# Kernel optimization log

Hardware: AMD Instinct MI355X
Metric: run time of the kernel (lower is better)

The kernel has to match this reference:

```python
import jax, jax.numpy as jnp
import numpy as np

HIDDEN = 2048
N_HEADS = 32
N_KV = 8
HEAD_DIM = HIDDEN // N_HEADS  # 64
GROUP = N_HEADS // N_KV       # 4
FFN = 8192
EPS = 1e-5
ROPE_BASE = 500000.0
NEG = -1e9


def rms_norm(x, w, eps=EPS):
    var = jnp.mean(x * x, axis=-1, keepdims=True)
    return x * jax.lax.rsqrt(var + eps) * w


def rope_cos_sin(position_ids):
    # inv_freq: [head_dim//2]
    inv_freq = 1.0 / (ROPE_BASE ** (jnp.arange(0, HEAD_DIM, 2, dtype=jnp.float32) / HEAD_DIM))
    freqs = position_ids.astype(jnp.float32)[:, :, None] * inv_freq[None, None, :]  # [b,s,d/2]
    emb = jnp.concatenate([freqs, freqs], axis=-1)  # [b,s,d]
    return jnp.cos(emb), jnp.sin(emb)


def rotate_half(x):
    x1, x2 = jnp.split(x, 2, axis=-1)
    return jnp.concatenate([-x2, x1], axis=-1)


def setup_inputs() -> dict:
    key = jax.random.key(0)
    ks = jax.random.split(key, 12)
    b, s = 2, 1024
    scale_h = 1.0 / np.sqrt(HIDDEN)
    scale_f = 1.0 / np.sqrt(FFN)
    hidden_states = jax.random.normal(ks[0], (b, s, HIDDEN), jnp.float32)
    causal = jnp.where(jnp.tril(jnp.ones((s, s), bool)), 0.0, NEG).astype(jnp.float32)
    attention_mask = jnp.broadcast_to(causal[None, None], (b, 1, s, s))
    position_ids = jnp.broadcast_to(jnp.arange(s, dtype=jnp.int32)[None], (b, s))
    return {
        "hidden_states": hidden_states,
        "attention_mask": attention_mask,
        "wq": jax.random.normal(ks[1], (HIDDEN, N_HEADS * HEAD_DIM), jnp.float32) * scale_h,
        "wk": jax.random.normal(ks[2], (HIDDEN, N_KV * HEAD_DIM), jnp.float32) * scale_h,
        "wv": jax.random.normal(ks[3], (HIDDEN, N_KV * HEAD_DIM), jnp.float32) * scale_h,
        "wo": jax.random.normal(ks[4], (N_HEADS * HEAD_DIM, HIDDEN), jnp.float32) * scale_h,
        "norm1_w": jnp.ones((HIDDEN,), jnp.float32),
        "norm2_w": jnp.ones((HIDDEN,), jnp.float32),
        "w_gate": jax.random.normal(ks[5], (HIDDEN, FFN), jnp.float32) * scale_h,
        "w_up": jax.random.normal(ks[6], (HIDDEN, FFN), jnp.float32) * scale_h,
        "w_down": jax.random.normal(ks[7], (FFN, HIDDEN), jnp.float32) * scale_f,
        "position_ids": position_ids,
    }


def reference(hidden_states, attention_mask, wq, wk, wv, wo, norm1_w, norm2_w,
              w_gate, w_up, w_down, position_ids):
    b, s, _ = hidden_states.shape
    residual = hidden_states
    normed = rms_norm(hidden_states, norm1_w)

    q = (normed @ wq).reshape(b, s, N_HEADS, HEAD_DIM).transpose(0, 2, 1, 3)  # [b,H,s,d]
    k = (normed @ wk).reshape(b, s, N_KV, HEAD_DIM).transpose(0, 2, 1, 3)    # [b,G,s,d]
    v = (normed @ wv).reshape(b, s, N_KV, HEAD_DIM).transpose(0, 2, 1, 3)

    cos, sin = rope_cos_sin(position_ids)  # [b,s,d]
    cos, sin = cos[:, None], sin[:, None]  # unsqueeze head dim
    q = q * cos + rotate_half(q) * sin
    k = k * cos + rotate_half(k) * sin

    # repeat_kv: [b,G,s,d] -> [b,H,s,d]
    k = jnp.repeat(k, GROUP, axis=1)
    v = jnp.repeat(v, GROUP, axis=1)

    scores = jnp.einsum('bhqd,bhkd->bhqk', q, k)
    scores = scores + attention_mask  # mask added BEFORE scaling, as in source
    attn = jax.nn.softmax(scores / np.sqrt(HEAD_DIM), axis=-1)
    ctx = jnp.einsum('bhqk,bhkd->bhqd', attn, v)
    ctx = ctx.transpose(0, 2, 1, 3).reshape(b, s, N_HEADS * HEAD_DIM)
    attn_out = ctx @ wo

    normed_ff = rms_norm(attn_out + residual, norm2_w)
    ff = (jax.nn.silu(normed_ff @ w_gate) * (normed_ff @ w_up)) @ w_down
    return attn_out + ff
```

## Files before the change

### kernel.cpp

```cpp
#include <hip/hip_runtime.h>
#include <hip/hip_bf16.h>
#include <cstddef>
#include <cstdint>

#define T_TOK   2048
#define HID     2048
#define NHEADS  32
#define NKV     8
#define HDIM    64
#define FFN_DIM 8192
#define QKV_N   3072

typedef __hip_bfloat16 bf16;
typedef __attribute__((ext_vector_type(8))) short short8;
typedef __attribute__((ext_vector_type(4))) float f32x4;
typedef __attribute__((ext_vector_type(4))) unsigned short us4;

typedef __attribute__((address_space(1))) const void cg_void;
typedef __attribute__((address_space(3))) void lds_void;

__global__ __launch_bounds__(256) void cast_transpose(const float* __restrict__ in,
                                                      bf16* __restrict__ out,
                                                      int K, int N)
{
    __shared__ bf16 t[64][65];
    const int n0 = blockIdx.x * 64, k0 = blockIdx.y * 64;
    const int tn = threadIdx.x & 63, tk = threadIdx.x >> 6;
    #pragma unroll
    for (int kk = tk; kk < 64; kk += 4)
        t[kk][tn] = __float2bfloat16(in[(size_t)(k0 + kk) * N + n0 + tn]);
    __syncthreads();
    #pragma unroll
    for (int nn = tk; nn < 64; nn += 4)
        out[(size_t)(n0 + nn) * K + k0 + tn] = t[tn][nn];
}

__global__ __launch_bounds__(256) void cast_ilv(const float* __restrict__ in,
                                                bf16* __restrict__ out,
                                                int N, int is_up)
{
    __shared__ bf16 t[64][65];
    const int n0 = blockIdx.x * 64, k0 = blockIdx.y * 64;
    const int tn = threadIdx.x & 63, tk = threadIdx.x >> 6;
    #pragma unroll
    for (int kk = tk; kk < 64; kk += 4)
        t[kk][tn] = __float2bfloat16(in[(size_t)(k0 + kk) * N + n0 + tn]);
    __syncthreads();
    #pragma unroll
    for (int nn = tk; nn < 64; nn += 4) {
        int n = n0 + nn;
        int r = ((n >> 5) << 6) + (is_up << 5) + (n & 31);
        out[(size_t)r * HID + k0 + tn] = t[tn][nn];
    }
}

__global__ __launch_bounds__(256) void rmsnorm_kernel(const float* __restrict__ x,
                                                      const float* __restrict__ w,
                                                      bf16* __restrict__ out)
{
    __shared__ float sm[4];
    const int row = blockIdx.x, tid = threadIdx.x;
    const float4* xr = (const float4*)(x + (size_t)row * HID);
    float4 a = xr[tid], b = xr[tid + 256];
    float ss = a.x*a.x + a.y*a.y + a.z*a.z + a.w*a.w
             + b.x*b.x + b.y*b.y + b.z*b.z + b.w*b.w;
    #pragma unroll
    for (int off = 32; off; off >>= 1) ss += __shfl_down(ss, off);
    if ((tid & 63) == 0) sm[tid >> 6] = ss;
    __syncthreads();
    float sc = rsqrtf((sm[0] + sm[1] + sm[2] + sm[3]) * (1.0f / HID) + 1e-5f);
    const float4* wr = (const float4*)w;
    float4 w0 = wr[tid], w1 = wr[tid + 256];
    bf16* o = out + (size_t)row * HID;
    o[tid*4+0] = __float2bfloat16(a.x * sc * w0.x);
    o[tid*4+1] = __float2bfloat16(a.y * sc * w0.y);
    o[tid*4+2] = __float2bfloat16(a.z * sc * w0.z);
    o[tid*4+3] = __float2bfloat16(a.w * sc * w0.w);
    o[1024+tid*4+0] = __float2bfloat16(b.x * sc * w1.x);
    o[1024+tid*4+1] = __float2bfloat16(b.y * sc * w1.y);
    o[1024+tid*4+2] = __float2bfloat16(b.z * sc * w1.z);
    o[1024+tid*4+3] = __float2bfloat16(b.w * sc * w1.w);
}

__global__ __launch_bounds__(256) void rmsnorm_add_kernel(const float* __restrict__ xa,
                                                          const float* __restrict__ xb,
                                                          const float* __restrict__ w,
                                                          bf16* __restrict__ out)
{
    __shared__ float sm[4];
    const int row = blockIdx.x, tid = threadIdx.x;
    const float4* ar = (const float4*)(xa + (size_t)row * HID);
    const float4* br = (const float4*)(xb + (size_t)row * HID);
    float4 a0 = ar[tid], a1 = ar[tid + 256];
    float4 b0 = br[tid], b1 = br[tid + 256];
    float4 s0, s1;
    s0.x = a0.x + b0.x; s0.y = a0.y + b0.y; s0.z = a0.z + b0.z; s0.w = a0.w + b0.w;
    s1.x = a1.x + b1.x; s1.y = a1.y + b1.y; s1.z = a1.z + b1.z; s1.w = a1.w + b1.w;
    float ss = s0.x*s0.x + s0.y*s0.y + s0.z*s0.z + s0.w*s0.w
             + s1.x*s1.x + s1.y*s1.y + s1.z*s1.z + s1.w*s1.w;
    #pragma unroll
    for (int off = 32; off; off >>= 1) ss += __shfl_down(ss, off);
    if ((tid & 63) == 0) sm[tid >> 6] = ss;
    __syncthreads();
    float sc = rsqrtf((sm[0] + sm[1] + sm[2] + sm[3]) * (1.0f / HID) + 1e-5f);
    const float4* wr = (const float4*)w;
    float4 w0 = wr[tid], w1 = wr[tid + 256];
    bf16* o = out + (size_t)row * HID;
    o[tid*4+0] = __float2bfloat16(s0.x * sc * w0.x);
    o[tid*4+1] = __float2bfloat16(s0.y * sc * w0.y);
    o[tid*4+2] = __float2bfloat16(s0.z * sc * w0.z);
    o[tid*4+3] = __float2bfloat16(s0.w * sc * w0.w);
    o[1024+tid*4+0] = __float2bfloat16(s1.x * sc * w1.x);
    o[1024+tid*4+1] = __float2bfloat16(s1.y * sc * w1.y);
    o[1024+tid*4+2] = __float2bfloat16(s1.z * sc * w1.z);
    o[1024+tid*4+3] = __float2bfloat16(s1.w * sc * w1.w);
}

template<int BN>
__device__ __forceinline__ void gemm_body(
    const bf16* __restrict__ A, const bf16* __restrict__ Bt,
    float* __restrict__ Cf,
    int lda, int kbeg, int klen, int ldc, int bx, int by)
{
    constexpr int NFR   = BN / 32;
    constexpr int CALLS = 4 + NFR;
    constexpr int KSRD  = 4 + NFR;
    __shared__ bf16 As[2 * 128 * 64];
    __shared__ bf16 Bs[2 * BN * 64];
    const int tid = threadIdx.x;
    const int wv = tid >> 6, ln = tid & 63;
    const int wr = wv >> 1, wc = wv & 1;
    const size_t m0 = (size_t)by * 128;
    const size_t n0 = (size_t)bx * BN;

    const int lrow = ln >> 3;
    const int lk   = (ln & 7) ^ lrow;

    const bf16* Abase = A  + (m0 + (size_t)wv*32 + lrow) * lda + kbeg + lk*8;
    const bf16* Bbase = Bt + (n0 + (size_t)wv*NFR*8 + lrow) * lda + kbeg + lk*8;
    bf16* AsW = As + wv*2048;
    bf16* BsW = Bs + wv*NFR*512;

    auto stage = [&](int p, int tk) {
        #pragma unroll
        for (int i = 0; i < 4; ++i)
            __builtin_amdgcn_global_load_lds((cg_void*)(Abase + (size_t)i*8*lda + tk),
                                             (lds_void*)(AsW + p*8192 + i*512), 16, 0, 0);
        #pragma unroll
        for (int i = 0; i < NFR; ++i)
            __builtin_amdgcn_global_load_lds((cg_void*)(Bbase + (size_t)i*8*lda + tk),
                                             (lds_void*)(BsW + p*(BN*64) + i*512), 16, 0, 0);
    };

    f32x4 acc[4][NFR] = {};
    const int nt = klen >> 6;

    stage(0, 0);
    stage(1, 64);
    asm volatile("s_waitcnt vmcnt(%0)" :: "n"(CALLS) : "memory");
    __builtin_amdgcn_sched_barrier(0);
    __builtin_amdgcn_s_barrier();

    for (int t = 0; t < nt; ++t) {
        const int p = t & 1;
        const char* Ab = (const char*)As + p * 16384;
        const char* Bb = (const char*)Bs + p * (BN * 128);

        short8 af[4][2], bfr[NFR][2];
        #pragma unroll
        for (int ks = 0; ks < 2; ++ks) {
            const int kbyte = ks*64 + (ln >> 4)*16;
            #pragma unroll
            for (int m = 0; m < 4; ++m) {
                int row = wr*64 + m*16 + (ln & 15);
                af[m][ks] = *(const short8*)(Ab + row*128 + (kbyte ^ ((row & 7) << 4)));
            }
            #pragma unroll
            for (int n = 0; n < NFR; ++n) {
                int row = wc*(BN/2) + n*16 + (ln & 15);
                bfr[n][ks] = *(const short8*)(Bb + row*128 + (kbyte ^ ((row & 7) << 4)));
            }
        }
        asm volatile("s_waitcnt lgkmcnt(%0)" :: "n"(KSRD) : "memory");
        __builtin_amdgcn_sched_barrier(0);
        __builtin_amdgcn_s_setprio(1);
        #pragma unroll
        for (int m = 0; m < 4; ++m)
            #pragma unroll
            for (int n = 0; n < NFR; ++n)
                acc[m][n] = __builtin_amdgcn_mfma_f32_16x16x32_bf16(af[m][0], bfr[n][0], acc[m][n], 0, 0, 0);
        __builtin_amdgcn_s_setprio(0);
        asm volatile("s_waitcnt lgkmcnt(0)" ::: "memory");
        __builtin_amdgcn_sched_barrier(0);
        __builtin_amdgcn_s_barrier();

        const bool more = (t + 2 < nt);
        if (more) stage(p, (t + 2) * 64);
        __builtin_amdgcn_sched_barrier(0);

        __builtin_amdgcn_s_setprio(1);
        #pragma unroll
        for (int m = 0; m < 4; ++m)
            #pragma unroll
            for (int n = 0; n < NFR; ++n)
                acc[m][n] = __builtin_amdgcn_mfma_f32_16x16x32_bf16(af[m][1], bfr[n][1], acc[m][n], 0, 0, 0);
        __builtin_amdgcn_s_setprio(0);

        if (more) { asm volatile("s_waitcnt vmcnt(%0)" :: "n"(CALLS) : "memory"); }
        else      { asm volatile("s_waitcnt vmcnt(0)" ::: "memory"); }
        __builtin_amdgcn_sched_barrier(0);
        __builtin_amdgcn_s_barrier();
    }

    const int cj = ln & 15, rj = ln >> 4;
    #pragma unroll
    for (int m = 0; m < 4; ++m) {
        #pragma unroll
        for (int j = 0; j < 4; ++j) {
            size_t row = m0 + wr*64 + m*16 + rj*4 + j;
            #pragma unroll
            for (int n = 0; n < NFR; ++n) {
                int col = (int)n0 + wc*(BN/2) + n*16 + cj;
                Cf[row * (size_t)ldc + col] = acc[m][n][j];
            }
        }
    }
}

__device__ __forceinline__ void swz(int& bx, int& by) {
    const int nwg = gridDim.x * gridDim.y;
    int orig = blockIdx.y * gridDim.x + blockIdx.x;
    int wg = (orig & 7) * (nwg >> 3) + (orig >> 3);
    by = wg % gridDim.y;
    bx = wg / gridDim.y;
}

__global__ __launch_bounds__(256) void g_qkv(const bf16* __restrict__ A,
                                             const bf16* __restrict__ Bt,
                                             float* __restrict__ C) {
    int bx, by; swz(bx, by);
    gemm_body<64>(A, Bt, C, HID, 0, HID, QKV_N, bx, by);
}
__global__ __launch_bounds__(256) void g_wo(const bf16* __restrict__ A,
                                            const bf16* __restrict__ Bt,
                                            float* __restrict__ C) {
    int bx, by; swz(bx, by);
    gemm_body<64>(A, Bt, C, HID, 0, HID, HID, bx, by);
}

template<int EPI>
__device__ __forceinline__ void gemm256_body(
    const bf16* __restrict__ A, const bf16* __restrict__ Bt,
    float* __restrict__ Cf, bf16* __restrict__ Cb,
    int lda, int kbeg, int klen, int ldc, int bx, int by)
{
    __shared__ bf16 As[2 * 256 * 64];
    __shared__ bf16 Bs[2 * 256 * 64];
    const int tid = threadIdx.x;
    const int wv = tid >> 6, ln = tid & 63;
    const int wr = wv >> 2, wc = wv & 3;
    const size_t m0 = (size_t)by * 256;
    const size_t n0 = (size_t)bx * 256;

    const int lrow = ln >> 3;
    const int lk   = (ln & 7) ^ lrow;

    const bf16* Abase = A  + (m0 + (size_t)wv*32 + lrow) * lda + kbeg + lk*8;
    const bf16* Bbase = Bt + (n0 + (size_t)wv*32 + lrow) * lda + kbeg + lk*8;
    bf16* AsW = As + wv*2048;
    bf16* BsW = Bs + wv*2048;

    auto stage = [&](int p, int tk) {
        #pragma unroll
        for (int i = 0; i < 4; ++i)
            __builtin_amdgcn_global_load_lds((cg_void*)(Abase + (size_t)i*8*lda + tk),
                                             (lds_void*)(AsW + p*16384 + i*512), 16, 0, 0);
        #pragma unroll
        for (int i = 0; i < 4; ++i)
            __builtin_amdgcn_global_load_lds((cg_void*)(Bbase + (size_t)i*8*lda + tk),
                                             (lds_void*)(BsW + p*16384 + i*512), 16, 0, 0);
    };

    f32x4 acc[8][4] = {};
    const int nt = klen >> 6;

    stage(0, 0);
    stage(1, 64);
    asm volatile("s_waitcnt vmcnt(8)" ::: "memory");
    __builtin_amdgcn_sched_barrier(0);
    __builtin_amdgcn_s_barrier();

    for (int t = 0; t < nt; ++t) {
        const int p = t & 1;
        const char* Ab = (const char*)As + p * 32768;
        const char* Bb = (const char*)Bs + p * 32768;

        short8 af0[8], bf0[4], af1[8], bf1[4];
        {
            const int kbyte = (ln >> 4) * 16;
            #pragma unroll
            for (int m = 0; m < 8; ++m) {
                int row = wr*128 + m*16 + (ln & 15);
                af0[m] = *(const short8*)(Ab + row*128 + (kbyte ^ ((row & 7) << 4)));
            }
            #pragma unroll
            for (int n = 0; n < 4; ++n) {
                int row = wc*64 + n*16 + (ln & 15);
                bf0[n] = *(const short8*)(Bb + row*128 + (kbyte ^ ((row & 7) << 4)));
            }
        }
        {
            const int kbyte = 64 + (ln >> 4) * 16;
            #pragma unroll
            for (int m = 0; m < 8; ++m) {
                int row = wr*128 + m*16 + (ln & 15);
                af1[m] = *(const short8*)(Ab + row*128 + (kbyte ^ ((row & 7) << 4)));
            }
            #pragma unroll
            for (int n = 0; n < 4; ++n) {
                int row = wc*64 + n*16 + (ln & 15);
                bf1[n] = *(const short8*)(Bb + row*128 + (kbyte ^ ((row & 7) << 4)));
            }
        }
        asm volatile("s_waitcnt lgkmcnt(12)" ::: "memory");
        __builtin_amdgcn_sched_barrier(0);
        __builtin_amdgcn_s_setprio(1);
        #pragma unroll
        for (int m = 0; m < 8; ++m)
            #pragma unroll
            for (int n = 0; n < 4; ++n)
                acc[m][n] = __builtin_amdgcn_mfma_f32_16x16x32_bf16(af0[m], bf0[n], acc[m][n], 0, 0, 0);
        __builtin_amdgcn_s_setprio(0);
        asm volatile("s_waitcnt lgkmcnt(0)" ::: "memory");
        __builtin_amdgcn_sched_barrier(0);
        __builtin_amdgcn_s_barrier();

        const bool more = (t + 2 < nt);
        if (more) stage(p, (t + 2) * 64);
        __builtin_amdgcn_sched_barrier(0);

        __builtin_amdgcn_s_setprio(1);
        #pragma unroll
        for (int m = 0; m < 8; ++m)
            #pragma unroll
            for (int n = 0; n < 4; ++n)
                acc[m][n] = __builtin_amdgcn_mfma_f32_16x16x32_bf16(af1[m], bf1[n], acc[m][n], 0, 0, 0);
        __builtin_amdgcn_s_setprio(0);

        if (more) { asm volatile("s_waitcnt vmcnt(8)" ::: "memory"); }
        else      { asm volatile("s_waitcnt vmcnt(0)" ::: "memory"); }
        __builtin_amdgcn_sched_barrier(0);
        __builtin_amdgcn_s_barrier();
    }

    const int cj = ln & 15, rj = ln >> 4;
    if constexpr (EPI == 4) {
        const int slab = (int)(n0 >> 6) + wc;
        #pragma unroll
        for (int m = 0; m < 8; ++m) {
            #pragma unroll
            for (int j = 0; j < 4; ++j) {
                size_t row = m0 + wr*128 + m*16 + rj*4 + j;
                #pragma unroll
                for (int n = 0; n < 2; ++n) {
                    int col = slab*32 + n*16 + cj;
                    float g = acc[m][n][j];
                    float u = acc[m][n+2][j];
                    Cb[row * (size_t)ldc + col] =
                        __float2bfloat16(g / (1.0f + __expf(-g)) * u);
                }
            }
        }
    } else {
        #pragma unroll
        for (int m = 0; m < 8; ++m) {
            #pragma unroll
            for (int j = 0; j < 4; ++j) {
                size_t row = m0 + wr*128 + m*16 + rj*4 + j;
                #pragma unroll
                for (int n = 0; n < 4; ++n) {
                    int col = (int)n0 + wc*64 + n*16 + cj;
                    unsafeAtomicAdd(&Cf[row * (size_t)ldc + col], acc[m][n][j]);
                }
            }
        }
    }
}

__global__ __launch_bounds__(512, 2) void g_gateup(const bf16* __restrict__ A,
                                                   const bf16* __restrict__ Bt,
                                                   bf16* __restrict__ C)
{
    const int nwg = gridDim.x * gridDim.y;
    int orig = blockIdx.y * gridDim.x + blockIdx.x;
    int wg = (orig & 7) * (nwg >> 3) + (orig >> 3);
    const int by = wg % gridDim.y, bx = wg / gridDim.y;
    gemm256_body<4>(A, Bt, nullptr, C, HID, 0, HID, FFN_DIM, bx, by);
}

__global__ __launch_bounds__(512, 2) void g_down(const bf16* __restrict__ A,
                                                 const bf16* __restrict__ Bt,
                                                 float* __restrict__ C)
{
    const int nwg = gridDim.x * gridDim.y;
    int orig = blockIdx.y * gridDim.x + blockIdx.x;
    int wg = (orig & 7) * (nwg >> 3) + (orig >> 3);
    const int by = wg % gridDim.y, bx = wg / gridDim.y;
    gemm256_body<5>(A, Bt, C, nullptr, FFN_DIM, blockIdx.z * 2048, 2048, HID, bx, by);
}

__global__ __launch_bounds__(256) void rope_cast(const float* __restrict__ qkv,
                                                 const int* __restrict__ pos_ids,
                                                 bf16* __restrict__ Qp,
                                                 bf16* __restrict__ Kp)
{
    const int t = blockIdx.x, tid = threadIdx.x;
    const int b = t >> 10, s = t & 1023;
    const float pos = (float)pos_ids[t];
    const float* row = qkv + (size_t)t * QKV_N;

    {
        int idx = tid * 4;
        int hq = idx >> 5, j = idx & 31;
        float xa[4], xb[4];
        *(float4*)xa = *(const float4*)(row + hq*64 + j);
        *(float4*)xb = *(const float4*)(row + hq*64 + j + 32);
        us4 o1, o2;
        #pragma unroll
        for (int jj = 0; jj < 4; ++jj) {
            float inv = exp2f(-(float)(j + jj) * 0.5916115177913804f);
            float ang = pos * inv, c, sn;
            sincosf(ang, &sn, &c);
            o1[jj] = __bfloat16_as_ushort(__float2bfloat16(xa[jj]*c - xb[jj]*sn));
            o2[jj] = __bfloat16_as_ushort(__float2bfloat16(xb[jj]*c + xa[jj]*sn));
        }
        bf16* qd = Qp + ((size_t)(b*32 + hq)*1024 + s)*64;
        *(us4*)(qd + j)      = o1;
        *(us4*)(qd + j + 32) = o2;
    }
    {
        int hk = tid >> 5, j = tid & 31;
        float a = row[2048 + hk*64 + j];
        float bb = row[2048 + hk*64 + j + 32];
        float inv = exp2f(-(float)j * 0.5916115177913804f);
        float ang = pos * inv, c, sn;
        sincosf(ang, &sn, &c);
        bf16* kd = Kp + ((size_t)(b*8 + hk)*1024 + s)*64;
        kd[j]      = __float2bfloat16(a*c - bb*sn);
        kd[j + 32] = __float2bfloat16(bb*c + a*sn);
    }
}

__global__ __launch_bounds__(256) void vt_cast(const float* __restrict__ qkv,
                                               bf16* __restrict__ Vt)
{
    __shared__ bf16 tile[64][64];
    const int s0 = blockIdx.x * 64;
    const int sec = blockIdx.y;
    const int b = sec >> 3, hk = sec & 7;
    const int tid = threadIdx.x;
    const float* base = qkv + ((size_t)(b*1024 + s0)) * QKV_N + 2560 + hk*64;
    const int srow = tid >> 2, d0 = (tid & 3) * 16;
    #pragma unroll
    for (int q = 0; q < 4; ++q) {
        float va[4];
        *(float4*)va = *(const float4*)(base + (size_t)srow * QKV_N + d0 + q*4);
        #pragma unroll
        for (int cc = 0; cc < 4; ++cc)
            tile[d0 + q*4 + cc][srow] = __float2bfloat16(va[cc]);
    }
    __syncthreads();
    const int dr = tid >> 2, sc = (tid & 3) * 16;
    bf16* od = Vt + ((size_t)sec*64 + dr)*1024 + s0 + sc;
    *(short8*)od       = *(const short8*)&tile[dr][sc];
    *(short8*)(od + 8) = *(const short8*)&tile[dr][sc + 8];
}

__global__ __launch_bounds__(256) void attn_mfma(const bf16* __restrict__ Qp,
                                                 const bf16* __restrict__ Kp,
                                                 const bf16* __restrict__ Vt,
                                                 bf16* __restrict__ ctx)
{
    __shared__ bf16 Ks[128 * 64];
    __shared__ bf16 Vs[64 * 128];
    __shared__ bf16 Ps[4 * 32 * 128];
    const int tid = threadIdx.x;
    const int w = tid >> 6, ln = tid & 63;
    const int qt = blockIdx.x, h = blockIdx.y, b = blockIdx.z;
    const int hk = h >> 2;
    const int q0 = qt * 128;

    const bf16* qsec = Qp + ((size_t)(b*32 + h)*1024 + q0 + w*32)*64;
    const bf16* ksec = Kp + ((size_t)(b*8 + hk)*1024)*64;
    const bf16* vsec = Vt + ((size_t)(b*8 + hk))*64*1024;

    short8 qf[2][2];
    #pragma unroll
    for (int f = 0; f < 2; ++f)
        #pragma unroll
        for (int kc = 0; kc < 2; ++kc)
            qf[f][kc] = *(const short8*)(qsec + (size_t)(f*16 + (ln & 15))*64 + kc*32 + (ln >> 4)*8);

    f32x4 acc_o[2][4] = {};
    f32x4 m[2], l[2];
    #pragma unroll
    for (int f = 0; f < 2; ++f)
        #pragma unroll
        for (int j = 0; j < 4; ++j) { m[f][j] = -1e30f; l[f][j] = 0.0f; }

    const int lrow = ln >> 3;
    const int lkk  = (ln & 7) ^ lrow;
    char* PsW = (char*)Ps + w * 8192;

    const int ntiles = qt + 1;
    for (int kt = 0; kt < ntiles; ++kt) {
        const int kv0 = kt * 128;
        {
            const bf16* kbase = ksec + (size_t)(kv0 + w*32 + lrow)*64 + lkk*8;
            bf16* KsW = Ks + w*2048;
            #pragma unroll
            for (int i = 0; i < 4; ++i)
                __builtin_amdgcn_global_load_lds((cg_void*)(kbase + (size_t)i*8*64),
                                                 (lds_void*)(KsW + i*512), 16, 0, 0);
        }
        {
            bf16* VsW = Vs + w*2048;
            #pragma unroll
            for (int i = 0; i < 4; ++i) {
                int d = w*16 + i*4 + (ln >> 4);
                __builtin_amdgcn_global_load_lds(
                    (cg_void*)(vsec + (size_t)d*1024 + kv0 + (((ln & 15) ^ (d & 7))*8)),
                    (lds_void*)(VsW + i*512), 16, 0, 0);
            }
        }
        __syncthreads();

        f32x4 acc_s[2][8] = {};
        #pragma unroll
        for (int c = 0; c < 8; ++c) {
            int kvr = c*16 + (ln & 15);
            const char* krow = (const char*)Ks + kvr*128;
            short8 kf0 = *(const short8*)(krow + (((ln >> 4)*16)      ^ ((kvr & 7) << 4)));
            short8 kf1 = *(const short8*)(krow + ((64 + (ln >> 4)*16) ^ ((kvr & 7) << 4)));
            #pragma unroll
            for (int f = 0; f < 2; ++f) {
                acc_s[f][c] = __builtin_amdgcn_mfma_f32_16x16x32_bf16(qf[f][0], kf0, acc_s[f][c], 0, 0, 0);
                acc_s[f][c] = __builtin_amdgcn_mfma_f32_16x16x32_bf16(qf[f][1], kf1, acc_s[f][c], 0, 0, 0);
            }
        }

        const bool diag = (kt == qt);
        f32x4 vmax[2];
        #pragma unroll
        for (int f = 0; f < 2; ++f)
            #pragma unroll
            for (int j = 0; j < 4; ++j) vmax[f][j] = -1e30f;
        #pragma unroll
        for (int f = 0; f < 2; ++f) {
            #pragma unroll
            for (int c = 0; c < 8; ++c) {
                f32x4 t = acc_s[f][c] * 0.125f;
                if (diag) {
                    int kv = kv0 + c*16 + (ln & 15);
                    int qg = q0 + w*32 + f*16 + (ln >> 4)*4;
                    #pragma unroll
                    for (int j = 0; j < 4; ++j)
                        if (kv > qg + j) t[j] = -1e30f;
                }
                acc_s[f][c] = t;
                #pragma unroll
                for (int j = 0; j < 4; ++j) vmax[f][j] = fmaxf(vmax[f][j], t[j]);
            }
            #pragma unroll
            for (int mk = 1; mk <= 8; mk <<= 1)
                #pragma unroll
                for (int j = 0; j < 4; ++j)
                    vmax[f][j] = fmaxf(vmax[f][j], __shfl_xor(vmax[f][j], mk));
        }

        #pragma unroll
        for (int f = 0; f < 2; ++f) {
            f32x4 r;
            #pragma unroll
            for (int j = 0; j < 4; ++j) {
                float mn = fmaxf(m[f][j], vmax[f][j]);
                r[j] = __expf(m[f][j] - mn);
                m[f][j] = mn;
                l[f][j] *= r[j];
            }
            #pragma unroll
            for (int df = 0; df < 4; ++df)
                #pragma unroll
                for (int j = 0; j < 4; ++j) acc_o[f][df][j] *= r[j];
        }

        f32x4 rs[2] = {};
        #pragma unroll
        for (int f = 0; f < 2; ++f) {
            #pragma unroll
            for (int c = 0; c < 8; ++c) {
                #pragma unroll
                for (int j = 0; j < 4; ++j) {
                    float p = __expf(acc_s[f][c][j] - m[f][j]);
                    rs[f][j] += p;
                    int qloc = f*16 + (ln >> 4)*4 + j;
                    int kvb  = (c*16 + (ln & 15))*2;
                    *(bf16*)(PsW + qloc*256 + (kvb ^ ((qloc & 7) << 4))) = __float2bfloat16(p);
                }
            }
            #pragma unroll
            for (int mk = 1; mk <= 8; mk <<= 1)
                #pragma unroll
                for (int j = 0; j < 4; ++j)
                    rs[f][j] += __shfl_xor(rs[f][j], mk);
            #pragma unroll
            for (int j = 0; j < 4; ++j) l[f][j] += rs[f][j];
        }

        #pragma unroll
        for (int kc = 0; kc < 4; ++kc) {
            short8 pa[2];
            #pragma unroll
            for (int f = 0; f < 2; ++f) {
                int qloc = f*16 + (ln & 15);
                pa[f] = *(const short8*)(PsW + qloc*256 + ((kc*64 + (ln >> 4)*16) ^ ((qloc & 7) << 4)));
            }
            #pragma unroll
            for (int df = 0; df < 4; ++df) {
                int dl = df*16 + (ln & 15);
                short8 vfr = *(const short8*)((const char*)Vs + dl*256 + ((kc*64 + (ln >> 4)*16) ^ ((dl & 7) << 4)));
                #pragma unroll
                for (int f = 0; f < 2; ++f)
                    acc_o[f][df] = __builtin_amdgcn_mfma_f32_16x16x32_bf16(pa[f], vfr, acc_o[f][df], 0, 0, 0);
            }
        }
        __syncthreads();
    }

    #pragma unroll
    for (int f = 0; f < 2; ++f) {
        f32x4 inv;
        #pragma unroll
        for (int j = 0; j < 4; ++j) inv[j] = 1.0f / l[f][j];
        #pragma unroll
        for (int df = 0; df < 4; ++df) {
            #pragma unroll
            for (int j = 0; j < 4; ++j) {
                int q = q0 + w*32 + f*16 + (ln >> 4)*4 + j;
                int d = df*16 + (ln & 15);
                ctx[((size_t)b*1024 + q)*HID + h*64 + d] = __float2bfloat16(acc_o[f][df][j] * inv[j]);
            }
        }
    }
}

extern "C" void kernel_launch(void* const* d_in, const int* in_sizes, int n_in,
                              void* d_out, int out_size, void* d_ws, size_t ws_size,
                              hipStream_t stream)
{
    const float* hidden = (const float*)d_in[0];
    const float* wq = (const float*)d_in[2];
    const float* wk = (const float*)d_in[3];
    const float* wv = (const float*)d_in[4];
    const float* wo = (const float*)d_in[5];
    const float* n1 = (const float*)d_in[6];
    const float* n2 = (const float*)d_in[7];
    const float* wg = (const float*)d_in[8];
    const float* wu = (const float*)d_in[9];
    const float* wd = (const float*)d_in[10];
    const int*  pos = (const int*)d_in[11];
    float* out = (float*)d_out;
    char* ws = (char*)d_ws;

    bf16* wgu_t  = (bf16*)(ws + 0);
    bf16* wd_t   = (bf16*)(ws + 67108864);
    bf16* wqkv_t = (bf16*)(ws + 100663296);
    bf16* wo_t   = (bf16*)(ws + 113246208);
    bf16* normed = (bf16*)(ws + 121634816);
    float* qkv   = (float*)(ws + 130023424);
    bf16* ctx    = (bf16*)(ws + 155189248);
    bf16* hb     = (bf16*)(ws + 130023424);
    bf16* Qp     = (bf16*)(ws + 121634816);
    bf16* Kp     = (bf16*)(ws + 163577856);
    bf16* Vt     = (bf16*)(ws + 165675008);

    cast_transpose<<<dim3(32, 32), 256, 0, stream>>>(wq, wqkv_t, 2048, 2048);
    cast_transpose<<<dim3(8, 32),  256, 0, stream>>>(wk, wqkv_t + 4194304, 2048, 512);
    cast_transpose<<<dim3(8, 32),  256, 0, stream>>>(wv, wqkv_t + 5242880, 2048, 512);
    cast_transpose<<<dim3(32, 32), 256, 0, stream>>>(wo, wo_t, 2048, 2048);
    cast_ilv<<<dim3(128, 32), 256, 0, stream>>>(wg, wgu_t, FFN_DIM, 0);
    cast_ilv<<<dim3(128, 32), 256, 0, stream>>>(wu, wgu_t, FFN_DIM, 1);
    cast_transpose<<<dim3(32, 128),256, 0, stream>>>(wd, wd_t, 8192, 2048);

    rmsnorm_kernel<<<T_TOK, 256, 0, stream>>>(hidden, n1, normed);
    g_qkv<<<dim3(QKV_N/64, T_TOK/128), 256, 0, stream>>>(normed, wqkv_t, qkv);
    rope_cast<<<T_TOK, 256, 0, stream>>>(qkv, pos, Qp, Kp);
    vt_cast<<<dim3(16, 16), 256, 0, stream>>>(qkv, Vt);
    attn_mfma<<<dim3(8, NHEADS, 2), 256, 0, stream>>>(Qp, Kp, Vt, ctx);
    g_wo<<<dim3(HID/64, T_TOK/128), 256, 0, stream>>>(ctx, wo_t, out);
    rmsnorm_add_kernel<<<T_TOK, 256, 0, stream>>>(out, hidden, n2, normed);
    g_gateup<<<dim3(16384/256, T_TOK/256), 512, 0, stream>>>(normed, wgu_t, hb);
    g_down<<<dim3(HID/256, T_TOK/256, 4), 512, 0, stream>>>(hb, wd_t, out);
}
```

Baseline: 511.4 us.

## Fuse RoPE and V transpose into QKV GEMM epilogue; vectorize weight cast kernels

The QKV projection GEMM is replaced by a fused kernel whose epilogue applies rotary embedding and writes bf16 Q and K in head-major layout, and writes V transposed. This removes the fp32 qkv intermediate and the separate rope_cast and vt_cast kernels along with their global round trip. The B-fragment column mapping is arranged so each wave holds the rotate-half partner columns. The weight cast/transpose kernels are also changed to use float4 loads and 4-wide packed bf16 stores. The epilogue performs many sincos calls and scattered 2-byte stores, which adds cost inside the GEMM.

```diff
diff --git a/kernel.cpp b/kernel.cpp
--- a/kernel.cpp
+++ b/kernel.cpp
@@ -23,34 +23,57 @@
                                                       bf16* __restrict__ out,
                                                       int K, int N)
 {
-    __shared__ bf16 t[64][65];
+    __shared__ bf16 t[64][68];
     const int n0 = blockIdx.x * 64, k0 = blockIdx.y * 64;
-    const int tn = threadIdx.x & 63, tk = threadIdx.x >> 6;
-    #pragma unroll
-    for (int kk = tk; kk < 64; kk += 4)
-        t[kk][tn] = __float2bfloat16(in[(size_t)(k0 + kk) * N + n0 + tn]);
+    const int g = threadIdx.x & 15, r = threadIdx.x >> 4;
+    #pragma unroll
+    for (int p = 0; p < 4; ++p) {
+        int kr = r + p*16;
+        float4 v = *(const float4*)(in + (size_t)(k0 + kr) * N + n0 + g*4);
+        t[kr][g*4+0] = __float2bfloat16(v.x);
+        t[kr][g*4+1] = __float2bfloat16(v.y);
+        t[kr][g*4+2] = __float2bfloat16(v.z);
+        t[kr][g*4+3] = __float2bfloat16(v.w);
+    }
     __syncthreads();
     #pragma unroll
-    for (int nn = tk; nn < 64; nn += 4)
-        out[(size_t)(n0 + nn) * K + k0 + tn] = t[tn][nn];
+    for (int p = 0; p < 4; ++p) {
+        int nr = r + p*16;
+        us4 pk;
+        #pragma unroll
+        for (int i = 0; i < 4; ++i)
+            pk[i] = __bfloat16_as_ushort(t[g*4+i][nr]);
+        *(us4*)(out + (size_t)(n0 + nr) * K + k0 + g*4) = pk;
+    }
 }
 
 __global__ __launch_bounds__(256) void cast_ilv(const float* __restrict__ in,
                                                 bf16* __restrict__ out,
                                                 int N, int is_up)
 {
-    __shared__ bf16 t[64][65];
+    __shared__ bf16 t[64][68];
     const int n0 = blockIdx.x * 64, k0 = blockIdx.y * 64;
-    const int tn = threadIdx.x & 63, tk = threadIdx.x >> 6;
-    #pragma unroll
-    for (int kk = tk; kk < 64; kk += 4)
-        t[kk][tn] = __float2bfloat16(in[(size_t)(k0 + kk) * N + n0 + tn]);
+    const int g = threadIdx.x & 15, r = threadIdx.x >> 4;
+    #pragma unroll
+    for (int p = 0; p < 4; ++p) {
+        int kr = r + p*16;
+        float4 v = *(const float4*)(in + (size_t)(k0 + kr) * N + n0 + g*4);
+        t[kr][g*4+0] = __float2bfloat16(v.x);
+        t[kr][g*4+1] = __float2bfloat16(v.y);
+        t[kr][g*4+2] = __float2bfloat16(v.z);
+        t[kr][g*4+3] = __float2bfloat16(v.w);
+    }
     __syncthreads();
     #pragma unroll
-    for (int nn = tk; nn < 64; nn += 4) {
-        int n = n0 + nn;
-        int r = ((n >> 5) << 6) + (is_up << 5) + (n & 31);
-        out[(size_t)r * HID + k0 + tn] = t[tn][nn];
+    for (int p = 0; p < 4; ++p) {
+        int nr = r + p*16;
+        int n = n0 + nr;
+        int rr = ((n >> 5) << 6) + (is_up << 5) + (n & 31);
+        us4 pk;
+        #pragma unroll
+        for (int i = 0; i < 4; ++i)
+            pk[i] = __bfloat16_as_ushort(t[g*4+i][nr]);
+        *(us4*)(out + (size_t)rr * HID + k0 + g*4) = pk;
     }
 }
 
@@ -235,17 +258,147 @@
     bx = wg / gridDim.y;
 }
 
-__global__ __launch_bounds__(256) void g_qkv(const bf16* __restrict__ A,
-                                             const bf16* __restrict__ Bt,
-                                             float* __restrict__ C) {
-    int bx, by; swz(bx, by);
-    gemm_body<64>(A, Bt, C, HID, 0, HID, QKV_N, bx, by);
-}
 __global__ __launch_bounds__(256) void g_wo(const bf16* __restrict__ A,
                                             const bf16* __restrict__ Bt,
                                             float* __restrict__ C) {
     int bx, by; swz(bx, by);
     gemm_body<64>(A, Bt, C, HID, 0, HID, HID, bx, by);
+}
+
+__global__ __launch_bounds__(256) void g_qkv_fused(const bf16* __restrict__ A,
+                                                   const bf16* __restrict__ Bt,
+                                                   const int* __restrict__ pos_ids,
+                                                   bf16* __restrict__ Qp,
+                                                   bf16* __restrict__ Kp,
+                                                   bf16* __restrict__ Vt)
+{
+    int bx, by; swz(bx, by);
+    __shared__ bf16 As[2 * 128 * 64];
+    __shared__ bf16 Bs[2 * 64 * 64];
+    const int tid = threadIdx.x;
+    const int wv = tid >> 6, ln = tid & 63;
+    const int wr = wv >> 1, wc = wv & 1;
+    const size_t m0 = (size_t)by * 128;
+    const size_t n0 = (size_t)bx * 64;
+
+    const int lrow = ln >> 3;
+    const int lk   = (ln & 7) ^ lrow;
+
+    const bf16* Abase = A  + (m0 + (size_t)wv*32 + lrow) * HID + lk*8;
+    const bf16* Bbase = Bt + (n0 + (size_t)wv*16 + lrow) * HID + lk*8;
+    bf16* AsW = As + wv*2048;
+    bf16* BsW = Bs + wv*1024;
+
+    auto stage = [&](int p, int tk) {
+        #pragma unroll
+        for (int i = 0; i < 4; ++i)
+            __builtin_amdgcn_global_load_lds((cg_void*)(Abase + (size_t)i*8*HID + tk),
+                                             (lds_void*)(AsW + p*8192 + i*512), 16, 0, 0);
+        #pragma unroll
+        for (int i = 0; i < 2; ++i)
+            __builtin_amdgcn_global_load_lds((cg_void*)(Bbase + (size_t)i*8*HID + tk),
+                                             (lds_void*)(BsW + p*4096 + i*512), 16, 0, 0);
+    };
+
+    f32x4 acc[4][2] = {};
+    const int nt = HID >> 6;
+
+    stage(0, 0);
+    stage(1, 64);
+    asm volatile("s_waitcnt vmcnt(6)" ::: "memory");
+    __builtin_amdgcn_sched_barrier(0);
+    __builtin_amdgcn_s_barrier();
+
+    for (int t = 0; t < nt; ++t) {
+        const int p = t & 1;
+        const char* Ab = (const char*)As + p * 16384;
+        const char* Bb = (const char*)Bs + p * 8192;
+
+        short8 af[4][2], bfr[2][2];
+        #pragma unroll
+        for (int ks = 0; ks < 2; ++ks) {
+            const int kbyte = ks*64 + (ln >> 4)*16;
+            #pragma unroll
+            for (int m = 0; m < 4; ++m) {
+                int row = wr*64 + m*16 + (ln & 15);
+                af[m][ks] = *(const short8*)(Ab + row*128 + (kbyte ^ ((row & 7) << 4)));
+            }
+            #pragma unroll
+            for (int n = 0; n < 2; ++n) {
+                int row = wc*16 + n*32 + (ln & 15);
+                bfr[n][ks] = *(const short8*)(Bb + row*128 + (kbyte ^ ((row & 7) << 4)));
+            }
+        }
+        asm volatile("s_waitcnt lgkmcnt(6)" ::: "memory");
+        __builtin_amdgcn_sched_barrier(0);
+        __builtin_amdgcn_s_setprio(1);
+        #pragma unroll
+        for (int m = 0; m < 4; ++m)
+            #pragma unroll
+            for (int n = 0; n < 2; ++n)
+                acc[m][n] = __builtin_amdgcn_mfma_f32_16x16x32_bf16(af[m][0], bfr[n][0], acc[m][n], 0, 0, 0);
+        __builtin_amdgcn_s_setprio(0);
+        asm volatile("s_waitcnt lgkmcnt(0)" ::: "memory");
+        __builtin_amdgcn_sched_barrier(0);
+        __builtin_amdgcn_s_barrier();
+
+        const bool more = (t + 2 < nt);
+        if (more) stage(p, (t + 2) * 64);
+        __builtin_amdgcn_sched_barrier(0);
+
+        __builtin_amdgcn_s_setprio(1);
+        #pragma unroll
+        for (int m = 0; m < 4; ++m)
+            #pragma unroll
+            for (int n = 0; n < 2; ++n)
+                acc[m][n] = __builtin_amdgcn_mfma_f32_16x16x32_bf16(af[m][1], bfr[n][1], acc[m][n], 0, 0, 0);
+        __builtin_amdgcn_s_setprio(0);
+
+        if (more) { asm volatile("s_waitcnt vmcnt(6)" ::: "memory"); }
+        else      { asm volatile("s_waitcnt vmcnt(0)" ::: "memory"); }
+        __builtin_amdgcn_sched_barrier(0);
+        __builtin_amdgcn_s_barrier();
+    }
+
+    const int rj = ln >> 4;
+    const int jj = wc*16 + (ln & 15);
+    if (bx < 40) {
+        const float invf = exp2f(-(float)jj * 0.5916115177913804f);
+        bf16* dst = (bx < 32) ? Qp : Kp;
+        const int hh = (bx < 32) ? bx : (bx - 32);
+        const int nh = (bx < 32) ? 32 : 8;
+        #pragma unroll
+        for (int m = 0; m < 4; ++m) {
+            #pragma unroll
+            for (int j = 0; j < 4; ++j) {
+                int t = (int)m0 + wr*64 + m*16 + rj*4 + j;
+                int s = t & 1023, b = t >> 10;
+                float ang = (float)pos_ids[t] * invf;
+                float c, sn;
+                sincosf(ang, &sn, &c);
+                float x1 = acc[m][0][j], x2 = acc[m][1][j];
+                size_t base = ((size_t)(b*nh + hh)*1024 + s)*64;
+                dst[base + jj]      = __float2bfloat16(x1*c - x2*sn);
+                dst[base + jj + 32] = __float2bfloat16(x2*c + x1*sn);
+            }
+        }
+    } else {
+        const int hv = bx - 40;
+        #pragma unroll
+        for (int m = 0; m < 4; ++m) {
+            int t0 = (int)m0 + wr*64 + m*16 + rj*4;
+            int s0 = t0 & 1023, b = t0 >> 10;
+            #pragma unroll
+            for (int n = 0; n < 2; ++n) {
+                int d = jj + n*32;
+                us4 pk;
+                #pragma unroll
+                for (int j = 0; j < 4; ++j)
+                    pk[j] = __bfloat16_as_ushort(__float2bfloat16(acc[m][n][j]));
+                *(us4*)(Vt + ((size_t)(b*8 + hv)*64 + d)*1024 + s0) = pk;
+            }
+        }
+    }
 }
 
 template<int EPI>
@@ -407,73 +560,6 @@
     int wg = (orig & 7) * (nwg >> 3) + (orig >> 3);
     const int by = wg % gridDim.y, bx = wg / gridDim.y;
     gemm256_body<5>(A, Bt, C, nullptr, FFN_DIM, blockIdx.z * 2048, 2048, HID, bx, by);
-}
-
-__global__ __launch_bounds__(256) void rope_cast(const float* __restrict__ qkv,
-                                                 const int* __restrict__ pos_ids,
-                                                 bf16* __restrict__ Qp,
-                                                 bf16* __restrict__ Kp)
-{
-    const int t = blockIdx.x, tid = threadIdx.x;
-    const int b = t >> 10, s = t & 1023;
-    const float pos = (float)pos_ids[t];
-    const float* row = qkv + (size_t)t * QKV_N;
-
-    {
-        int idx = tid * 4;
-        int hq = idx >> 5, j = idx & 31;
-        float xa[4], xb[4];
-        *(float4*)xa = *(const float4*)(row + hq*64 + j);
-        *(float4*)xb = *(const float4*)(row + hq*64 + j + 32);
-        us4 o1, o2;
-        #pragma unroll
-        for (int jj = 0; jj < 4; ++jj) {
-            float inv = exp2f(-(float)(j + jj) * 0.5916115177913804f);
-            float ang = pos * inv, c, sn;
-            sincosf(ang, &sn, &c);
-            o1[jj] = __bfloat16_as_ushort(__float2bfloat16(xa[jj]*c - xb[jj]*sn));
-            o2[jj] = __bfloat16_as_ushort(__float2bfloat16(xb[jj]*c + xa[jj]*sn));
-        }
-        bf16* qd = Qp + ((size_t)(b*32 + hq)*1024 + s)*64;
-        *(us4*)(qd + j)      = o1;
-        *(us4*)(qd + j + 32) = o2;
-    }
-    {
-        int hk = tid >> 5, j = tid & 31;
-        float a = row[2048 + hk*64 + j];
-        float bb = row[2048 + hk*64 + j + 32];
-        float inv = exp2f(-(float)j * 0.5916115177913804f);
-        float ang = pos * inv, c, sn;
-        sincosf(ang, &sn, &c);
-        bf16* kd = Kp + ((size_t)(b*8 + hk)*1024 + s)*64;
-        kd[j]      = __float2bfloat16(a*c - bb*sn);
-        kd[j + 32] = __float2bfloat16(bb*c + a*sn);
-    }
-}
-
-__global__ __launch_bounds__(256) void vt_cast(const float* __restrict__ qkv,
-                                               bf16* __restrict__ Vt)
-{
-    __shared__ bf16 tile[64][64];
-    const int s0 = blockIdx.x * 64;
-    const int sec = blockIdx.y;
-    const int b = sec >> 3, hk = sec & 7;
-    const int tid = threadIdx.x;
-    const float* base = qkv + ((size_t)(b*1024 + s0)) * QKV_N + 2560 + hk*64;
-    const int srow = tid >> 2, d0 = (tid & 3) * 16;
-    #pragma unroll
-    for (int q = 0; q < 4; ++q) {
-        float va[4];
-        *(float4*)va = *(const float4*)(base + (size_t)srow * QKV_N + d0 + q*4);
-        #pragma unroll
-        for (int cc = 0; cc < 4; ++cc)
-            tile[d0 + q*4 + cc][srow] = __float2bfloat16(va[cc]);
-    }
-    __syncthreads();
-    const int dr = tid >> 2, sc = (tid & 3) * 16;
-    bf16* od = Vt + ((size_t)sec*64 + dr)*1024 + s0 + sc;
-    *(short8*)od       = *(const short8*)&tile[dr][sc];
-    *(short8*)(od + 8) = *(const short8*)&tile[dr][sc + 8];
 }
 
 __global__ __launch_bounds__(256) void attn_mfma(const bf16* __restrict__ Qp,
@@ -677,10 +763,9 @@
     bf16* wqkv_t = (bf16*)(ws + 100663296);
     bf16* wo_t   = (bf16*)(ws + 113246208);
     bf16* normed = (bf16*)(ws + 121634816);
-    float* qkv   = (float*)(ws + 130023424);
+    bf16* Qp     = (bf16*)(ws + 130023424);
     bf16* ctx    = (bf16*)(ws + 155189248);
     bf16* hb     = (bf16*)(ws + 130023424);
-    bf16* Qp     = (bf16*)(ws + 121634816);
     bf16* Kp     = (bf16*)(ws + 163577856);
     bf16* Vt     = (bf16*)(ws + 165675008);
 
@@ -693,9 +778,8 @@
     cast_transpose<<<dim3(32, 128),256, 0, stream>>>(wd, wd_t, 8192, 2048);
 
     rmsnorm_kernel<<<T_TOK, 256, 0, stream>>>(hidden, n1, normed);
-    g_qkv<<<dim3(QKV_N/64, T_TOK/128), 256, 0, stream>>>(normed, wqkv_t, qkv);
-    rope_cast<<<T_TOK, 256, 0, stream>>>(qkv, pos, Qp, Kp);
-    vt_cast<<<dim3(16, 16), 256, 0, stream>>>(qkv, Vt);
+    g_qkv_fused<<<dim3(QKV_N/64, T_TOK/128), 256, 0, stream>>>(
+        normed, wqkv_t, pos, Qp, Kp, Vt);
     attn_mfma<<<dim3(8, NHEADS, 2), 256, 0, stream>>>(Qp, Kp, Vt, ctx);
     g_wo<<<dim3(HID/64, T_TOK/128), 256, 0, stream>>>(ctx, wo_t, out);
     rmsnorm_add_kernel<<<T_TOK, 256, 0, stream>>>(out, hidden, n2, normed);
```

After: 478.9 us, median of 2. -6.3%, faster.
